# Kernel tuning notes

Hardware: AMD Instinct MI355X
Metric: run time of the kernel (lower is better)

Reference implementation:

```python
import jax, jax.numpy as jnp
import numpy as np
import math

N, T, D, H = 64, 256, 768, 256

def setup_inputs() -> dict:
    key = jax.random.key(0)
    ks = jax.random.split(key, 5)
    s = 0.02
    return {
        "x": jax.random.normal(ks[0], (N, T, D), dtype=jnp.float32),
        "Wq": jax.random.normal(ks[1], (H, D), dtype=jnp.float32) * s,
        "Wk": jax.random.normal(ks[2], (H, D), dtype=jnp.float32) * s,
        "Wv": jax.random.normal(ks[3], (H, D), dtype=jnp.float32) * s,
        "Wo": jax.random.normal(ks[4], (D, H), dtype=jnp.float32) * s,
    }

def reference(x, Wq, Wk, Wv, Wo):
    # flatten [N,T,D] -> [M,D], full self-attention over all M tokens
    n, t, d = x.shape
    xf = x.reshape(n * t, d)                      # [M, D]
    q = xf @ Wq.T                                  # [M, H]
    k = xf @ Wk.T                                  # [M, H]
    v = xf @ Wv.T                                  # [M, H]
    scale = 1.0 / math.sqrt(q.shape[-1])
    att = jax.nn.softmax((q @ k.T) * scale, axis=-1)  # [M, M]
    pooled = (att @ v) @ Wo.T                      # [M, D]
    return pooled.mean(axis=0, keepdims=True)      # [1, D]
```

## Files before the change

### kernel.cpp

```cpp
#include <hip/hip_runtime.h>


typedef unsigned short u16;
typedef __attribute__((ext_vector_type(8))) unsigned short u16x8;
typedef __bf16 bf16x8 __attribute__((ext_vector_type(8)));
typedef float f32x4 __attribute__((ext_vector_type(4)));

#define MTOK 16384
#define DDIM 768
#define HDIM 256
#define SM_SCALE 0.0625f

#define OFF_XB    (size_t)0
#define OFF_WCAT  (size_t)25165824
#define OFF_QB    (size_t)26345472
#define OFF_KB    (size_t)34734080
#define OFF_VF    (size_t)43122688
#define OFF_RS    (size_t)59899904
#define OFF_RINV  (size_t)59965440
#define OFF_CA    (size_t)60030976
#define OFF_P     (size_t)60096512
#define WS_NEED   (size_t)60097536

__device__ __forceinline__ u16 f2bf(float f) {
  union { float f; unsigned u; } v; v.f = f;
  unsigned r = v.u + 0x7fffu + ((v.u >> 16) & 1u);
  return (u16)(r >> 16);
}

__global__ void k_conv(const float* __restrict__ src, u16* __restrict__ dst, int n8) {
  int i = blockIdx.x * blockDim.x + threadIdx.x;
  if (i >= n8) return;
  const float4* s = (const float4*)src;
  float4 a = s[2 * i], b = s[2 * i + 1];
  u16x8 o = { f2bf(a.x), f2bf(a.y), f2bf(a.z), f2bf(a.w),
              f2bf(b.x), f2bf(b.y), f2bf(b.z), f2bf(b.w) };
  *(u16x8*)(dst + (size_t)i * 8) = o;
}

__device__ __forceinline__ void stage_tile(const u16* __restrict__ g, int ld,
                                           u16* lds, int wid, int lane) {
  const int r = lane >> 2;
  const int c = (lane & 3) * 8;
#pragma unroll
  for (int i = 0; i < 2; ++i) {
    int ii = wid * 2 + i;
    const u16* gp = g + (size_t)(ii * 16 + r) * ld + c;
    __builtin_amdgcn_global_load_lds(
        (const __attribute__((address_space(1))) unsigned int*)gp,
        (__attribute__((address_space(3))) unsigned int*)(lds + ii * 512),
        16, 0, 0);
  }
}

#define KSTEP(APTR, LDA, BPTR, LDB)                                           \
  {                                                                           \
    stage_tile((APTR), (LDA), As, wid, lane);                                 \
    stage_tile((BPTR), (LDB), Bs, wid, lane);                                 \
    __syncthreads();                                                          \
    bf16x8 af[4], bfr[4];                                                     \
    const int kk = (lane >> 4) * 8;                                           \
    _Pragma("unroll") for (int m = 0; m < 4; ++m)                             \
        af[m] = *(const bf16x8*)(As + (wm * 64 + m * 16 + (lane & 15)) * 32 + kk); \
    _Pragma("unroll") for (int n = 0; n < 4; ++n)                             \
        bfr[n] = *(const bf16x8*)(Bs + (wn * 64 + n * 16 + (lane & 15)) * 32 + kk); \
    _Pragma("unroll") for (int m = 0; m < 4; ++m)                             \
        _Pragma("unroll") for (int n = 0; n < 4; ++n)                         \
            acc[m][n] = __builtin_amdgcn_mfma_f32_16x16x32_bf16(              \
                af[m], bfr[n], acc[m][n], 0, 0, 0);                           \
    __syncthreads();                                                          \
  }

__global__ __launch_bounds__(256, 2) void k_qkv(const u16* __restrict__ Xb,
                                                const u16* __restrict__ Wcat,
                                                u16* __restrict__ Qb,
                                                u16* __restrict__ Kb,
                                                float* __restrict__ Vf) {
  __shared__ u16 As[128 * 32];
  __shared__ u16 Bs[128 * 32];
  const int tid = threadIdx.x, wid = tid >> 6, lane = tid & 63;
  const int wm = wid >> 1, wn = wid & 1;
  const int row0 = blockIdx.x * 128;
  const int col0 = blockIdx.y * 128;
  f32x4 acc[4][4] = {};
  for (int k0 = 0; k0 < DDIM; k0 += 32) {
    KSTEP(Xb + (size_t)row0 * DDIM + k0, DDIM,
          Wcat + (size_t)col0 * DDIM + k0, DDIM);
  }
#pragma unroll
  for (int m = 0; m < 4; ++m)
#pragma unroll
    for (int n = 0; n < 4; ++n) {
      int col = col0 + wn * 64 + n * 16 + (lane & 15);
#pragma unroll
      for (int j = 0; j < 4; ++j) {
        int row = row0 + wm * 64 + m * 16 + (lane >> 4) * 4 + j;
        float v = acc[m][n][j];
        if (col < 256)      Qb[(size_t)row * HDIM + col]         = f2bf(v);
        else if (col < 512) Kb[(size_t)row * HDIM + (col - 256)] = f2bf(v);
        else                Vf[(size_t)row * HDIM + (col - 512)] = v;
      }
    }
}

__global__ __launch_bounds__(256, 2) void k_pass1(const u16* __restrict__ Qb,
                                                  const u16* __restrict__ Kb,
                                                  float* __restrict__ rowsum) {
  __shared__ u16 As[128 * 32];
  __shared__ u16 Bs[128 * 32];
  const int tid = threadIdx.x, wid = tid >> 6, lane = tid & 63;
  const int wm = wid >> 1, wn = wid & 1;
  const int rowA = blockIdx.x * 128;
  const int jg = blockIdx.y;
  float es[4][4] = {};
  for (int it = 0; it < 16; ++it) {
    const int rowB = (jg * 16 + it) * 128;
    f32x4 acc[4][4] = {};
    for (int k0 = 0; k0 < HDIM; k0 += 32) {
      KSTEP(Qb + (size_t)rowA * HDIM + k0, HDIM,
            Kb + (size_t)rowB * HDIM + k0, HDIM);
    }
#pragma unroll
    for (int m = 0; m < 4; ++m)
#pragma unroll
      for (int n = 0; n < 4; ++n)
#pragma unroll
        for (int j = 0; j < 4; ++j)
          es[m][j] += __expf(acc[m][n][j] * SM_SCALE);
  }
#pragma unroll
  for (int m = 0; m < 4; ++m)
#pragma unroll
    for (int j = 0; j < 4; ++j) {
      float v = es[m][j];
      v += __shfl_xor(v, 1);  v += __shfl_xor(v, 2);
      v += __shfl_xor(v, 4);  v += __shfl_xor(v, 8);
      if ((lane & 15) == 0)
        atomicAdd(&rowsum[rowA + wm * 64 + m * 16 + (lane >> 4) * 4 + j], v);
    }
}

__global__ void k_rinv(const float* __restrict__ rowsum, float* __restrict__ rinv) {
  int i = blockIdx.x * 256 + threadIdx.x;
  if (i < MTOK) rinv[i] = 1.0f / (rowsum[i] * (float)MTOK);
}

__global__ __launch_bounds__(256, 2) void k_pass2(const u16* __restrict__ Qb,
                                                  const u16* __restrict__ Kb,
                                                  const float* __restrict__ rinv,
                                                  float* __restrict__ colacc) {
  __shared__ u16 As[128 * 32];
  __shared__ u16 Bs[128 * 32];
  const int tid = threadIdx.x, wid = tid >> 6, lane = tid & 63;
  const int wm = wid >> 1, wn = wid & 1;
  const int rowA = blockIdx.x * 128;
  const int rowB = blockIdx.y * 128;
  f32x4 acc[4][4] = {};
  for (int k0 = 0; k0 < HDIM; k0 += 32) {
    KSTEP(Qb + (size_t)rowA * HDIM + k0, HDIM,
          Kb + (size_t)rowB * HDIM + k0, HDIM);
  }
  float r16[4][4];
#pragma unroll
  for (int m = 0; m < 4; ++m)
#pragma unroll
    for (int j = 0; j < 4; ++j)
      r16[m][j] = rinv[rowA + wm * 64 + m * 16 + (lane >> 4) * 4 + j];
  float cs[4] = {};
#pragma unroll
  for (int m = 0; m < 4; ++m)
#pragma unroll
    for (int n = 0; n < 4; ++n)
#pragma unroll
      for (int j = 0; j < 4; ++j)
        cs[n] += __expf(acc[m][n][j] * SM_SCALE) * r16[m][j];
#pragma unroll
  for (int n = 0; n < 4; ++n) {
    float v = cs[n];
    v += __shfl_xor(v, 16);  v += __shfl_xor(v, 32);
    if ((lane >> 4) == 0)
      atomicAdd(&colacc[rowB + wn * 64 + n * 16 + (lane & 15)], v);
  }
}

__global__ void k_p(const float* __restrict__ colacc, const float* __restrict__ Vf,
                    float* __restrict__ p) {
  const int h = threadIdx.x;
  const int r0 = blockIdx.x * 128;
  float s = 0.f;
  for (int r = r0; r < r0 + 128; ++r)
    s += colacc[r] * Vf[(size_t)r * HDIM + h];
  atomicAdd(&p[h], s);
}

__global__ void k_out(const float* __restrict__ p, const float* __restrict__ Wo,
                      float* __restrict__ out) {
  const int d = blockIdx.x * 256 + threadIdx.x;
  if (d >= DDIM) return;
  float s = 0.f;
  for (int h = 0; h < HDIM; ++h) s += p[h] * Wo[(size_t)d * HDIM + h];
  out[d] = s;
}

extern "C" void kernel_launch(void* const* d_in, const int* in_sizes, int n_in,
                              void* d_out, int out_size, void* d_ws, size_t ws_size,
                              hipStream_t stream) {
  const float* x  = (const float*)d_in[0];
  const float* Wq = (const float*)d_in[1];
  const float* Wk = (const float*)d_in[2];
  const float* Wv = (const float*)d_in[3];
  const float* Wo = (const float*)d_in[4];
  float* out = (float*)d_out;

  char* ws = (char*)d_ws;
  u16*   Xb     = (u16*)(ws + OFF_XB);
  u16*   Wcat   = (u16*)(ws + OFF_WCAT);
  u16*   Qb     = (u16*)(ws + OFF_QB);
  u16*   Kb     = (u16*)(ws + OFF_KB);
  float* Vf     = (float*)(ws + OFF_VF);
  float* rowsum = (float*)(ws + OFF_RS);
  float* rinv   = (float*)(ws + OFF_RINV);
  float* colacc = (float*)(ws + OFF_CA);
  float* p      = (float*)(ws + OFF_P);

  k_conv<<<(MTOK * DDIM / 8 + 255) / 256, 256, 0, stream>>>(x, Xb, MTOK * DDIM / 8);
  const int w8 = HDIM * DDIM / 8;
  k_conv<<<(w8 + 255) / 256, 256, 0, stream>>>(Wq, Wcat + 0 * HDIM * DDIM, w8);
  k_conv<<<(w8 + 255) / 256, 256, 0, stream>>>(Wk, Wcat + 1 * HDIM * DDIM, w8);
  k_conv<<<(w8 + 255) / 256, 256, 0, stream>>>(Wv, Wcat + 2 * HDIM * DDIM, w8);

  hipMemsetAsync(ws + OFF_RS, 0, WS_NEED - OFF_RS, stream);

  k_qkv<<<dim3(MTOK / 128, DDIM / 128), 256, 0, stream>>>(Xb, Wcat, Qb, Kb, Vf);

  k_pass1<<<dim3(MTOK / 128, 8), 256, 0, stream>>>(Qb, Kb, rowsum);
  k_rinv<<<MTOK / 256, 256, 0, stream>>>(rowsum, rinv);

  k_pass2<<<dim3(MTOK / 128, MTOK / 128), 256, 0, stream>>>(Qb, Kb, rinv, colacc);

  k_p<<<MTOK / 128, 256, 0, stream>>>(colacc, Vf, p);
  k_out<<<(DDIM + 255) / 256, 256, 0, stream>>>(p, Wo, out);
}
```

Baseline: 487.6 us.

## Replace score passes with 256x256-tile, LDS double-buffered direct-load kernel

Merges the two QK^T softmax passes into one templated kernel. Each 512-thread block owns a 256-row Q panel and sweeps 8 K tiles of 256 columns. Operands stream through swizzled, double-buffered shared memory using global_load_lds direct loads, with the next K-slice prefetched while MFMAs run on the current one. The larger tiles and the pipelining aim to cut global re-reads of Q/K and hide load latency behind compute. In exchange it needs 128KB of LDS per block, which limits occupancy and adds register pressure from 32 accumulators per lane.

```diff
diff --git a/kernel.cpp b/kernel.cpp
--- a/kernel.cpp
+++ b/kernel.cpp
@@ -103,84 +103,156 @@
     }
 }
 
-__global__ __launch_bounds__(256, 2) void k_pass1(const u16* __restrict__ Qb,
+
+__device__ __forceinline__ void stage_kt(u16* sh, const u16* __restrict__ Qb,
+                                         const u16* __restrict__ Kb,
+                                         int rp, int cg, int wid, int srow,
+                                         int wsrc, int t) {
+  const int kb = (t & 3) * 128;
+  u16* dst = sh + (t & 1) * 32768;
+  if (wid < 4) {
+    const char* base = (const char*)Qb + (size_t)(rp * 256) * 512 + kb + wsrc;
+#pragma unroll
+    for (int j = 0; j < 8; ++j) {
+      int c = wid * 8 + j;
+      int row = c * 8 + srow;
+      __builtin_amdgcn_global_load_lds(
+          (const __attribute__((address_space(1))) unsigned int*)(base + (size_t)row * 512),
+          (__attribute__((address_space(3))) unsigned int*)(dst + c * 512),
+          16, 0, 0);
+    }
+  } else {
+    const int ct = cg * 8 + (t >> 2);
+    const char* base = (const char*)Kb + (size_t)(ct * 256) * 512 + kb + wsrc;
+#pragma unroll
+    for (int j = 0; j < 8; ++j) {
+      int c = (wid - 4) * 8 + j;
+      int row = c * 8 + srow;
+      __builtin_amdgcn_global_load_lds(
+          (const __attribute__((address_space(1))) unsigned int*)(base + (size_t)row * 512),
+          (__attribute__((address_space(3))) unsigned int*)(dst + 16384 + c * 512),
+          16, 0, 0);
+    }
+  }
+}
+
+template <int PASS>
+__global__ __launch_bounds__(512, 2) void k_spass(const u16* __restrict__ Qb,
                                                   const u16* __restrict__ Kb,
-                                                  float* __restrict__ rowsum) {
-  __shared__ u16 As[128 * 32];
-  __shared__ u16 Bs[128 * 32];
+                                                  const float* __restrict__ rinv,
+                                                  float* __restrict__ dst) {
+  __shared__ u16 sh[65536];
   const int tid = threadIdx.x, wid = tid >> 6, lane = tid & 63;
-  const int wm = wid >> 1, wn = wid & 1;
-  const int rowA = blockIdx.x * 128;
-  const int jg = blockIdx.y;
-  float es[4][4] = {};
-  for (int it = 0; it < 16; ++it) {
-    const int rowB = (jg * 16 + it) * 128;
-    f32x4 acc[4][4] = {};
-    for (int k0 = 0; k0 < HDIM; k0 += 32) {
-      KSTEP(Qb + (size_t)rowA * HDIM + k0, HDIM,
-            Kb + (size_t)rowB * HDIM + k0, HDIM);
-    }
-#pragma unroll
-    for (int m = 0; m < 4; ++m)
-#pragma unroll
-      for (int n = 0; n < 4; ++n)
-#pragma unroll
-        for (int j = 0; j < 4; ++j)
-          es[m][j] += __expf(acc[m][n][j] * SM_SCALE);
-  }
-#pragma unroll
-  for (int m = 0; m < 4; ++m)
-#pragma unroll
-    for (int j = 0; j < 4; ++j) {
-      float v = es[m][j];
-      v += __shfl_xor(v, 1);  v += __shfl_xor(v, 2);
-      v += __shfl_xor(v, 4);  v += __shfl_xor(v, 8);
-      if ((lane & 15) == 0)
-        atomicAdd(&rowsum[rowA + wm * 64 + m * 16 + (lane >> 4) * 4 + j], v);
-    }
+  const int wm = wid >> 2, wn = wid & 3;
+  const int rp = blockIdx.x >> 3;
+  const int cg = blockIdx.x & 7;
+
+  const int colp = (lane >> 4) * 16;
+  const int swzr = (lane & 7) << 4;
+  const int rd0 = ((0  + colp) ^ swzr) >> 1;
+  const int rd1 = ((64 + colp) ^ swzr) >> 1;
+  const int srow = lane >> 3;
+  const int wsrc = ((lane & 7) ^ srow) << 4;
+
+  f32x4 acc[8][4] = {};
+  float aux[8][4];
+#pragma unroll
+  for (int mi = 0; mi < 8; ++mi)
+#pragma unroll
+    for (int j = 0; j < 4; ++j)
+      aux[mi][j] = (PASS == 1) ? 0.0f
+          : rinv[rp * 256 + wm * 128 + mi * 16 + (lane >> 4) * 4 + j];
+
+  stage_kt(sh, Qb, Kb, rp, cg, wid, srow, wsrc, 0);
+
+  for (int t = 0; t < 32; ++t) {
+    if (t + 1 < 32) {
+      stage_kt(sh, Qb, Kb, rp, cg, wid, srow, wsrc, t + 1);
+      asm volatile("s_waitcnt vmcnt(8)" ::: "memory");
+    } else {
+      asm volatile("s_waitcnt vmcnt(0)" ::: "memory");
+    }
+    __builtin_amdgcn_s_barrier();
+
+    const int base = (t & 1) * 32768;
+    const u16* Ab = sh + base;
+    const u16* Bb = sh + base + 16384;
+
+    bf16x8 bq[4][2];
+#pragma unroll
+    for (int ni = 0; ni < 4; ++ni) {
+      const int rb = (wn * 64 + ni * 16 + (lane & 15)) * 64;
+      bq[ni][0] = *(const bf16x8*)(Bb + rb + rd0);
+      bq[ni][1] = *(const bf16x8*)(Bb + rb + rd1);
+    }
+    __builtin_amdgcn_s_setprio(1);
+#pragma unroll
+    for (int mi = 0; mi < 8; ++mi) {
+      const int ra = (wm * 128 + mi * 16 + (lane & 15)) * 64;
+      bf16x8 a0 = *(const bf16x8*)(Ab + ra + rd0);
+      bf16x8 a1 = *(const bf16x8*)(Ab + ra + rd1);
+#pragma unroll
+      for (int ni = 0; ni < 4; ++ni) {
+        acc[mi][ni] = __builtin_amdgcn_mfma_f32_16x16x32_bf16(a0, bq[ni][0], acc[mi][ni], 0, 0, 0);
+        acc[mi][ni] = __builtin_amdgcn_mfma_f32_16x16x32_bf16(a1, bq[ni][1], acc[mi][ni], 0, 0, 0);
+      }
+    }
+    __builtin_amdgcn_s_setprio(0);
+    __builtin_amdgcn_s_barrier();
+
+    if ((t & 3) == 3) {
+      if (PASS == 1) {
+#pragma unroll
+        for (int mi = 0; mi < 8; ++mi)
+#pragma unroll
+          for (int ni = 0; ni < 4; ++ni)
+#pragma unroll
+            for (int j = 0; j < 4; ++j)
+              aux[mi][j] += __expf(acc[mi][ni][j] * SM_SCALE);
+      } else {
+        const int ct = cg * 8 + (t >> 2);
+        float cs[4] = {};
+#pragma unroll
+        for (int mi = 0; mi < 8; ++mi)
+#pragma unroll
+          for (int ni = 0; ni < 4; ++ni)
+#pragma unroll
+            for (int j = 0; j < 4; ++j)
+              cs[ni] += __expf(acc[mi][ni][j] * SM_SCALE) * aux[mi][j];
+#pragma unroll
+        for (int ni = 0; ni < 4; ++ni) {
+          float v = cs[ni];
+          v += __shfl_xor(v, 16);
+          v += __shfl_xor(v, 32);
+          if ((lane >> 4) == 0)
+            atomicAdd(&dst[ct * 256 + wn * 64 + ni * 16 + (lane & 15)], v);
+        }
+      }
+#pragma unroll
+      for (int mi = 0; mi < 8; ++mi)
+#pragma unroll
+        for (int ni = 0; ni < 4; ++ni)
+          acc[mi][ni] = (f32x4){0.f, 0.f, 0.f, 0.f};
+    }
+  }
+
+  if (PASS == 1) {
+#pragma unroll
+    for (int mi = 0; mi < 8; ++mi)
+#pragma unroll
+      for (int j = 0; j < 4; ++j) {
+        float v = aux[mi][j];
+        v += __shfl_xor(v, 1);  v += __shfl_xor(v, 2);
+        v += __shfl_xor(v, 4);  v += __shfl_xor(v, 8);
+        if ((lane & 15) == 0)
+          atomicAdd(&dst[rp * 256 + wm * 128 + mi * 16 + (lane >> 4) * 4 + j], v);
+      }
+  }
 }
 
 __global__ void k_rinv(const float* __restrict__ rowsum, float* __restrict__ rinv) {
   int i = blockIdx.x * 256 + threadIdx.x;
   if (i < MTOK) rinv[i] = 1.0f / (rowsum[i] * (float)MTOK);
-}
-
-__global__ __launch_bounds__(256, 2) void k_pass2(const u16* __restrict__ Qb,
-                                                  const u16* __restrict__ Kb,
-                                                  const float* __restrict__ rinv,
-                                                  float* __restrict__ colacc) {
-  __shared__ u16 As[128 * 32];
-  __shared__ u16 Bs[128 * 32];
-  const int tid = threadIdx.x, wid = tid >> 6, lane = tid & 63;
-  const int wm = wid >> 1, wn = wid & 1;
-  const int rowA = blockIdx.x * 128;
-  const int rowB = blockIdx.y * 128;
-  f32x4 acc[4][4] = {};
-  for (int k0 = 0; k0 < HDIM; k0 += 32) {
-    KSTEP(Qb + (size_t)rowA * HDIM + k0, HDIM,
-          Kb + (size_t)rowB * HDIM + k0, HDIM);
-  }
-  float r16[4][4];
-#pragma unroll
-  for (int m = 0; m < 4; ++m)
-#pragma unroll
-    for (int j = 0; j < 4; ++j)
-      r16[m][j] = rinv[rowA + wm * 64 + m * 16 + (lane >> 4) * 4 + j];
-  float cs[4] = {};
-#pragma unroll
-  for (int m = 0; m < 4; ++m)
-#pragma unroll
-    for (int n = 0; n < 4; ++n)
-#pragma unroll
-      for (int j = 0; j < 4; ++j)
-        cs[n] += __expf(acc[m][n][j] * SM_SCALE) * r16[m][j];
-#pragma unroll
-  for (int n = 0; n < 4; ++n) {
-    float v = cs[n];
-    v += __shfl_xor(v, 16);  v += __shfl_xor(v, 32);
-    if ((lane >> 4) == 0)
-      atomicAdd(&colacc[rowB + wn * 64 + n * 16 + (lane & 15)], v);
-  }
 }
 
 __global__ void k_p(const float* __restrict__ colacc, const float* __restrict__ Vf,
@@ -233,10 +305,9 @@
 
   k_qkv<<<dim3(MTOK / 128, DDIM / 128), 256, 0, stream>>>(Xb, Wcat, Qb, Kb, Vf);
 
-  k_pass1<<<dim3(MTOK / 128, 8), 256, 0, stream>>>(Qb, Kb, rowsum);
+  k_spass<1><<<512, 512, 0, stream>>>(Qb, Kb, nullptr, rowsum);
   k_rinv<<<MTOK / 256, 256, 0, stream>>>(rowsum, rinv);
-
-  k_pass2<<<dim3(MTOK / 128, MTOK / 128), 256, 0, stream>>>(Qb, Kb, rinv, colacc);
+  k_spass<2><<<512, 512, 0, stream>>>(Qb, Kb, rinv, colacc);
 
   k_p<<<MTOK / 128, 256, 0, stream>>>(colacc, Vf, p);
   k_out<<<(DDIM + 255) / 256, 256, 0, stream>>>(p, Wo, out);
```

After: 536.5 us. 10.0% more time.
